# Kernel tuning notes

Hardware: AMD Instinct MI355X
Metric: run time of the kernel (lower is better)

## Reference

```python
import jax, jax.numpy as jnp
import numpy as np

NUM_USERS = 1_000_000
NUM_ITEMS = 100_000
NUM_BINS = 32
NUM_FREQ_TABLES = 50
EMB_DIM = 64
BATCH = 2_097_152


def setup_inputs() -> dict:
    key = jax.random.key(0)
    k1, k2, k3, k4, k5, k6, k7 = jax.random.split(key, 7)
    user = jax.random.randint(k1, (BATCH,), 0, NUM_USERS, dtype=jnp.int32)
    item = jax.random.randint(k2, (BATCH,), 0, NUM_ITEMS, dtype=jnp.int32)
    freq = jax.random.randint(k3, (BATCH,), 0, NUM_BINS, dtype=jnp.int32)
    idx_emb = jax.random.randint(k4, (BATCH,), 0, NUM_FREQ_TABLES, dtype=jnp.int32)
    zero = jnp.zeros((BATCH,), dtype=jnp.int32)
    # learned parameters (init matches torch: normal(0, 0.1) for bias/user/item, zeros for freq tables)
    bias_w = 0.1 * jax.random.normal(k5, (1, 1), dtype=jnp.float32)
    user_w = 0.1 * jax.random.normal(k6, (NUM_USERS, EMB_DIM), dtype=jnp.float32)
    item_w = 0.1 * jax.random.normal(k7, (NUM_ITEMS, EMB_DIM), dtype=jnp.float32)
    freq_w = jnp.zeros((NUM_FREQ_TABLES, NUM_BINS, 1), dtype=jnp.float32)
    return {"user": user, "item": item, "freq": freq, "idx_emb": idx_emb,
            "zero": zero, "bias_w": bias_w, "user_w": user_w,
            "item_w": item_w, "freq_w": freq_w}


def reference(user, item, freq, idx_emb, zero, bias_w, user_w, item_w, freq_w):
    # bias lookup: [B]
    bias = bias_w[zero, 0]
    # per-sample dot product between user and item embeddings: [B]
    u = user_w[user]            # [B, D]
    v = item_w[item]            # [B, D]
    dot = jnp.einsum('bd,bd->b', u, v)
    # per-sample frequency lookup: table chosen by idx_emb, bin by freq -> [B]
    # (replaces the torch per-sample Python loop with one fused gather)
    fe = freq_w[idx_emb, freq, 0]
    return bias + dot + fe
```

## Files before the change

### kernel.cpp

```cpp
#include <hip/hip_runtime.h>


#define EMB_DIM 64

__global__ __launch_bounds__(256) void sfc_fwd(
    const int* __restrict__ user, const int* __restrict__ item,
    const int* __restrict__ freq, const int* __restrict__ idx_emb,
    const int* __restrict__ zero, const float* __restrict__ bias_w,
    const float* __restrict__ user_w, const float* __restrict__ item_w,
    const float* __restrict__ freq_w, float* __restrict__ out, int B)
{
    const int group_in_block = threadIdx.x >> 4;
    const int lane = threadIdx.x & 15;
    const int groups_per_grid = (gridDim.x * blockDim.x) >> 4;

    for (int s = blockIdx.x * 16 + group_in_block; s < B; s += groups_per_grid) {
        const int u_idx = user[s];
        const int i_idx = item[s];

        const float4 uv = *reinterpret_cast<const float4*>(
            user_w + (size_t)u_idx * EMB_DIM + lane * 4);
        const float4 vv = *reinterpret_cast<const float4*>(
            item_w + (size_t)i_idx * EMB_DIM + lane * 4);

        float d = uv.x * vv.x + uv.y * vv.y + uv.z * vv.z + uv.w * vv.w;

        d += __shfl_xor(d, 1);
        d += __shfl_xor(d, 2);
        d += __shfl_xor(d, 4);
        d += __shfl_xor(d, 8);

        if (lane == 0) {
            const float bias = bias_w[zero[s]];
            const float fe   = freq_w[idx_emb[s] * 32 + freq[s]];
            out[s] = bias + d + fe;
        }
    }
}

extern "C" void kernel_launch(void* const* d_in, const int* in_sizes, int n_in,
                              void* d_out, int out_size, void* d_ws, size_t ws_size,
                              hipStream_t stream) {
    const int B = in_sizes[0];
    const int*   user    = (const int*)d_in[0];
    const int*   item    = (const int*)d_in[1];
    const int*   freq    = (const int*)d_in[2];
    const int*   idx_emb = (const int*)d_in[3];
    const int*   zero    = (const int*)d_in[4];
    const float* bias_w  = (const float*)d_in[5];
    const float* user_w  = (const float*)d_in[6];
    const float* item_w  = (const float*)d_in[7];
    const float* freq_w  = (const float*)d_in[8];
    float* out = (float*)d_out;

    const int blocks = 2048;
    sfc_fwd<<<blocks, 256, 0, stream>>>(user, item, freq, idx_emb, zero,
                                        bias_w, user_w, item_w, freq_w, out, B);
}
```

Measured before the change: 165.7 us.

## Bucket samples by user index before gathering embeddings for locality

Adds a counting-sort pipeline (init, histogram, scan, scatter) that groups samples by user index bucket into a workspace array of packed records. The main kernel then processes bucketed samples so user-table gathers hit nearby rows and share cache, and it interleaves chunks across blocks. This trades extra passes over the index arrays, atomics, and a scattered output write for better locality on the 256 MB user table. The old direct kernel is kept as a fallback when the workspace is too small. Bias is read from bias_w[0] instead of through the zero index, which assumes the bias table has a single row.

Result: slower. 329.8 us (+99.0%).

```diff
diff --git a/kernel.cpp b/kernel.cpp
--- a/kernel.cpp
+++ b/kernel.cpp
@@ -2,39 +2,118 @@
 
 
 #define EMB_DIM 64
+#define NB 8192
+#define BUCKET_SHIFT 7
 
-__global__ __launch_bounds__(256) void sfc_fwd(
+__global__ void k_init(int* __restrict__ cnt, int* __restrict__ cursor) {
+    int i = blockIdx.x * blockDim.x + threadIdx.x;
+    if (i < NB) { cnt[i] = 0; cursor[i] = 0; }
+}
+
+__global__ void k_hist(const int* __restrict__ user, int* __restrict__ cnt, int B) {
+    int i = blockIdx.x * blockDim.x + threadIdx.x;
+    int stride = gridDim.x * blockDim.x;
+    for (int s = i; s < B; s += stride)
+        atomicAdd(&cnt[user[s] >> BUCKET_SHIFT], 1);
+}
+
+__global__ __launch_bounds__(1024) void k_scan(const int* __restrict__ cnt,
+                                               int* __restrict__ base) {
+    __shared__ int part[1024];
+    const int t = threadIdx.x;
+    int loc[8];
+    int sum = 0;
+#pragma unroll
+    for (int j = 0; j < 8; ++j) { loc[j] = cnt[t * 8 + j]; sum += loc[j]; }
+    part[t] = sum;
+    __syncthreads();
+    for (int off = 1; off < 1024; off <<= 1) {
+        int v = (t >= off) ? part[t - off] : 0;
+        __syncthreads();
+        part[t] += v;
+        __syncthreads();
+    }
+    int excl = part[t] - sum;
+#pragma unroll
+    for (int j = 0; j < 8; ++j) { base[t * 8 + j] = excl; excl += loc[j]; }
+}
+
+__global__ void k_scatter(const int* __restrict__ user, const int* __restrict__ item,
+                          const int* __restrict__ freq, const int* __restrict__ idx_emb,
+                          const int* __restrict__ base, int* __restrict__ cursor,
+                          int4* __restrict__ pairs, int B) {
+    int i = blockIdx.x * blockDim.x + threadIdx.x;
+    int stride = gridDim.x * blockDim.x;
+    for (int s = i; s < B; s += stride) {
+        const int u = user[s];
+        const int b = u >> BUCKET_SHIFT;
+        const int pos = atomicAdd(&cursor[b], 1);
+        const unsigned packed = (unsigned)s | ((unsigned)freq[s] << 21)
+                              | ((unsigned)idx_emb[s] << 26);
+        pairs[base[b] + pos] = make_int4(u, item[s], (int)packed, 0);
+    }
+}
+
+__global__ __launch_bounds__(256) void k_main(
+    const int4* __restrict__ pairs, const float* __restrict__ bias_w,
+    const float* __restrict__ user_w, const float* __restrict__ item_w,
+    const float* __restrict__ freq_w, float* __restrict__ out, int B, int nchunks)
+{
+    __shared__ int4 sp[256];
+    const int b = blockIdx.x;
+    const int chunk = ((nchunks & 7) == 0) ? ((b & 7) * (nchunks >> 3) + (b >> 3)) : b;
+    const int tid = threadIdx.x;
+    const int s0 = chunk * 256;
+    {
+        const int idx = s0 + tid;
+        sp[tid] = (idx < B) ? pairs[idx] : make_int4(0, 0, 0, 0);
+    }
+    __syncthreads();
+    const float bias0 = bias_w[0];
+    const int g = tid >> 4, lane = tid & 15;
+
+#pragma unroll
+    for (int j = 0; j < 16; j += 2) {
+        if (s0 + g * 16 + j >= B) break;
+        const int4 p0 = sp[g * 16 + j];
+        const int4 p1 = sp[g * 16 + j + 1];
+        const float4 u0 = *reinterpret_cast<const float4*>(user_w + (size_t)p0.x * EMB_DIM + lane * 4);
+        const float4 v0 = *reinterpret_cast<const float4*>(item_w + (size_t)p0.y * EMB_DIM + lane * 4);
+        const float4 u1 = *reinterpret_cast<const float4*>(user_w + (size_t)p1.x * EMB_DIM + lane * 4);
+        const float4 v1 = *reinterpret_cast<const float4*>(item_w + (size_t)p1.y * EMB_DIM + lane * 4);
+        float d0 = u0.x * v0.x + u0.y * v0.y + u0.z * v0.z + u0.w * v0.w;
+        float d1 = u1.x * v1.x + u1.y * v1.y + u1.z * v1.z + u1.w * v1.w;
+        d0 += __shfl_xor(d0, 1); d0 += __shfl_xor(d0, 2); d0 += __shfl_xor(d0, 4); d0 += __shfl_xor(d0, 8);
+        d1 += __shfl_xor(d1, 1); d1 += __shfl_xor(d1, 2); d1 += __shfl_xor(d1, 4); d1 += __shfl_xor(d1, 8);
+        if (lane == 0) {
+            const unsigned q0 = (unsigned)p0.z, q1 = (unsigned)p1.z;
+            const int sA = (int)(q0 & 0x1FFFFFu), sB = (int)(q1 & 0x1FFFFFu);
+            const float fe0 = freq_w[((q0 >> 26) & 63u) * 32 + ((q0 >> 21) & 31u)];
+            const float fe1 = freq_w[((q1 >> 26) & 63u) * 32 + ((q1 >> 21) & 31u)];
+            const int last = s0 + g * 16 + j + 1;
+            out[sA] = bias0 + d0 + fe0;
+            if (last < B) out[sB] = bias0 + d1 + fe1;
+        }
+    }
+}
+
+__global__ __launch_bounds__(256) void sfc_direct(
     const int* __restrict__ user, const int* __restrict__ item,
     const int* __restrict__ freq, const int* __restrict__ idx_emb,
     const int* __restrict__ zero, const float* __restrict__ bias_w,
     const float* __restrict__ user_w, const float* __restrict__ item_w,
     const float* __restrict__ freq_w, float* __restrict__ out, int B)
 {
-    const int group_in_block = threadIdx.x >> 4;
+    const int group = threadIdx.x >> 4;
     const int lane = threadIdx.x & 15;
-    const int groups_per_grid = (gridDim.x * blockDim.x) >> 4;
-
-    for (int s = blockIdx.x * 16 + group_in_block; s < B; s += groups_per_grid) {
-        const int u_idx = user[s];
-        const int i_idx = item[s];
-
-        const float4 uv = *reinterpret_cast<const float4*>(
-            user_w + (size_t)u_idx * EMB_DIM + lane * 4);
-        const float4 vv = *reinterpret_cast<const float4*>(
-            item_w + (size_t)i_idx * EMB_DIM + lane * 4);
-
+    const int stride = (gridDim.x * blockDim.x) >> 4;
+    for (int s = blockIdx.x * 16 + group; s < B; s += stride) {
+        const float4 uv = *reinterpret_cast<const float4*>(user_w + (size_t)user[s] * EMB_DIM + lane * 4);
+        const float4 vv = *reinterpret_cast<const float4*>(item_w + (size_t)item[s] * EMB_DIM + lane * 4);
         float d = uv.x * vv.x + uv.y * vv.y + uv.z * vv.z + uv.w * vv.w;
-
-        d += __shfl_xor(d, 1);
-        d += __shfl_xor(d, 2);
-        d += __shfl_xor(d, 4);
-        d += __shfl_xor(d, 8);
-
-        if (lane == 0) {
-            const float bias = bias_w[zero[s]];
-            const float fe   = freq_w[idx_emb[s] * 32 + freq[s]];
-            out[s] = bias + d + fe;
-        }
+        d += __shfl_xor(d, 1); d += __shfl_xor(d, 2); d += __shfl_xor(d, 4); d += __shfl_xor(d, 8);
+        if (lane == 0)
+            out[s] = bias_w[zero[s]] + d + freq_w[idx_emb[s] * 32 + freq[s]];
     }
 }
 
@@ -53,7 +132,23 @@
     const float* freq_w  = (const float*)d_in[8];
     float* out = (float*)d_out;
 
-    const int blocks = 2048;
-    sfc_fwd<<<blocks, 256, 0, stream>>>(user, item, freq, idx_emb, zero,
-                                        bias_w, user_w, item_w, freq_w, out, B);
+    char* w = (char*)d_ws;
+    int*  cnt    = (int*)(w);
+    int*  cursor = (int*)(w + 32 * 1024);
+    int*  base   = (int*)(w + 64 * 1024);
+    int4* pairs  = (int4*)(w + (1 << 20));
+    const size_t need = (size_t)(1 << 20) + (size_t)B * sizeof(int4);
+
+    if (ws_size < need) {
+        sfc_direct<<<2048, 256, 0, stream>>>(user, item, freq, idx_emb, zero,
+                                             bias_w, user_w, item_w, freq_w, out, B);
+        return;
+    }
+
+    const int nchunks = (B + 255) / 256;
+    k_init<<<(NB + 255) / 256, 256, 0, stream>>>(cnt, cursor);
+    k_hist<<<1024, 256, 0, stream>>>(user, cnt, B);
+    k_scan<<<1, 1024, 0, stream>>>(cnt, base);
+    k_scatter<<<2048, 256, 0, stream>>>(user, item, freq, idx_emb, base, cursor, pairs, B);
+    k_main<<<nchunks, 256, 0, stream>>>(pairs, bias_w, user_w, item_w, freq_w, out, B, nchunks);
 }
```

## Split user-table gathers into two index-range passes for cache locality

Applied to the files above, without the earlier changes.

Launches the kernel twice, and each pass handles only the samples whose user index falls in half of the user table. The goal is to keep each pass's user-embedding working set small enough to stay resident in the last-level cache. It also reads the single bias value once per thread instead of gathering through the zero index array. In exchange, the user index array is scanned twice, and about half the groups idle in each pass. User rows are reused only about twice on average, so there may be little locality to recover.

After: 263.7 us. +59.1%, slower.

```diff
diff --git a/kernel.cpp b/kernel.cpp
--- a/kernel.cpp
+++ b/kernel.cpp
@@ -3,37 +3,33 @@
 
 #define EMB_DIM 64
 
-__global__ __launch_bounds__(256) void sfc_fwd(
+__global__ __launch_bounds__(256) void sfc_pass(
     const int* __restrict__ user, const int* __restrict__ item,
     const int* __restrict__ freq, const int* __restrict__ idx_emb,
-    const int* __restrict__ zero, const float* __restrict__ bias_w,
-    const float* __restrict__ user_w, const float* __restrict__ item_w,
-    const float* __restrict__ freq_w, float* __restrict__ out, int B)
+    const float* __restrict__ bias_w, const float* __restrict__ user_w,
+    const float* __restrict__ item_w, const float* __restrict__ freq_w,
+    float* __restrict__ out, int B, int lo, int hi)
 {
-    const int group_in_block = threadIdx.x >> 4;
-    const int lane = threadIdx.x & 15;
-    const int groups_per_grid = (gridDim.x * blockDim.x) >> 4;
+    const int group  = threadIdx.x >> 4;
+    const int lane   = threadIdx.x & 15;
+    const int stride = (gridDim.x * blockDim.x) >> 4;
+    const float bias0 = bias_w[0];
 
-    for (int s = blockIdx.x * 16 + group_in_block; s < B; s += groups_per_grid) {
-        const int u_idx = user[s];
-        const int i_idx = item[s];
-
-        const float4 uv = *reinterpret_cast<const float4*>(
-            user_w + (size_t)u_idx * EMB_DIM + lane * 4);
-        const float4 vv = *reinterpret_cast<const float4*>(
-            item_w + (size_t)i_idx * EMB_DIM + lane * 4);
-
-        float d = uv.x * vv.x + uv.y * vv.y + uv.z * vv.z + uv.w * vv.w;
-
-        d += __shfl_xor(d, 1);
-        d += __shfl_xor(d, 2);
-        d += __shfl_xor(d, 4);
-        d += __shfl_xor(d, 8);
-
-        if (lane == 0) {
-            const float bias = bias_w[zero[s]];
-            const float fe   = freq_w[idx_emb[s] * 32 + freq[s]];
-            out[s] = bias + d + fe;
+    for (int s = blockIdx.x * 16 + group; s < B; s += stride) {
+        const int u = user[s];
+        if (u >= lo && u < hi) {
+            const float4 uv = *reinterpret_cast<const float4*>(
+                user_w + (size_t)u * EMB_DIM + lane * 4);
+            const float4 vv = *reinterpret_cast<const float4*>(
+                item_w + (size_t)item[s] * EMB_DIM + lane * 4);
+            float d = uv.x * vv.x + uv.y * vv.y + uv.z * vv.z + uv.w * vv.w;
+            d += __shfl_xor(d, 1);
+            d += __shfl_xor(d, 2);
+            d += __shfl_xor(d, 4);
+            d += __shfl_xor(d, 8);
+            if (lane == 0) {
+                out[s] = bias0 + d + freq_w[idx_emb[s] * 32 + freq[s]];
+            }
         }
     }
 }
@@ -46,14 +42,21 @@
     const int*   item    = (const int*)d_in[1];
     const int*   freq    = (const int*)d_in[2];
     const int*   idx_emb = (const int*)d_in[3];
-    const int*   zero    = (const int*)d_in[4];
     const float* bias_w  = (const float*)d_in[5];
     const float* user_w  = (const float*)d_in[6];
     const float* item_w  = (const float*)d_in[7];
     const float* freq_w  = (const float*)d_in[8];
     float* out = (float*)d_out;
 
-    const int blocks = 2048;
-    sfc_fwd<<<blocks, 256, 0, stream>>>(user, item, freq, idx_emb, zero,
-                                        bias_w, user_w, item_w, freq_w, out, B);
+    const int num_users = in_sizes[6] / EMB_DIM;
+    const int NPASS = 2;
+    const int span = (num_users + NPASS - 1) / NPASS;
+
+    for (int p = 0; p < NPASS; ++p) {
+        const int lo = p * span;
+        const int hi = (p == NPASS - 1) ? 0x7FFFFFFF : (p + 1) * span;
+        sfc_pass<<<2048, 256, 0, stream>>>(user, item, freq, idx_emb,
+                                           bias_w, user_w, item_w, freq_w,
+                                           out, B, lo, hi);
+    }
 }
```
